# Performance work log

Hardware: AMD Instinct MI355X
Metric: run time of the kernel (lower is better)

Reference implementation:

```python
import jax, jax.numpy as jnp
import numpy as np

M = 1536   # rows (users)
N = 1536   # cols (items)
P_ROW = 4  # Chebyshev order over rows
P_COL = 4  # Chebyshev order over cols
OUT = 32   # out_channels_GCCN


def cheb_basis(L, order):
    """Stack of Chebyshev polynomials T_k(L), shape (order+1, n, n)."""
    n = L.shape[0]
    Ts = [jnp.eye(n, dtype=L.dtype)]
    if order > 0:
        Ts.append(L)
    for _ in range(2, order + 1):
        Ts.append(2.0 * (L @ Ts[-1]) - Ts[-2])
    return jnp.stack(Ts)


def setup_inputs() -> dict:
    key = jax.random.key(0)
    kx, kr, kc, kt = jax.random.split(key, 4)
    x = jax.random.normal(kx, (1, M, N), dtype=jnp.float32)
    # Scaled symmetric 'Laplacians' with spectral radius < 1 so the
    # Chebyshev recursion stays numerically stable.
    Ar = jax.random.normal(kr, (M, M), dtype=jnp.float32)
    Lr = (Ar + Ar.T) / (4.0 * jnp.sqrt(jnp.float32(M)))
    Ac = jax.random.normal(kc, (N, N), dtype=jnp.float32)
    Lc = (Ac + Ac.T) / (4.0 * jnp.sqrt(jnp.float32(N)))
    theta = jax.random.normal(kt, (P_ROW + 1, P_COL + 1, 1, OUT), dtype=jnp.float32) * 0.05
    bias = jnp.zeros((OUT,), dtype=jnp.float32)
    return {"x": x, "Lr": Lr, "Lc": Lc, "theta": theta, "bias": bias}


def reference(x, Lr, Lc, theta, bias):
    # Chebyshev bases: Tr (p_row+1, M, M), Tc (p_col+1, N, N)
    Tr = cheb_basis(Lr, theta.shape[0] - 1)
    Tc = cheb_basis(Lc, theta.shape[1] - 1)
    # Stage 1: row transform -> (i, c, M, N)
    x_row = jnp.einsum('imp,cpn->icmn', Tr, x)
    # Stage 2: col transform -> (i, j, c, M, N)
    basis_feats = jnp.einsum('icmn,jnk->ijcmk', x_row, Tc)
    # Stage 3: bilinear weights -> (OUT, M, N)
    out = jnp.einsum('ijcmn,ijco->omn', basis_feats, theta)
    return out + bias[:, None, None]
```

## Files before the change

kernel.cpp:

```cpp
#include <hip/hip_runtime.h>
#include <hip/hip_bf16.h>


#define NDIM 1536
#define PM (NDIM * NDIM)
#define NK 24

typedef __attribute__((ext_vector_type(8))) short bf16x8;
typedef __attribute__((ext_vector_type(4))) float f32x4;

__device__ inline void gload_lds16(const void* g, void* l) {
  __builtin_amdgcn_global_load_lds(
      (const __attribute__((address_space(1))) void*)g,
      (__attribute__((address_space(3))) void*)l, 16, 0, 0);
}

__device__ inline unsigned short f2bf(float f) {
  __hip_bfloat16 h = __float2bfloat16(f);
  return *reinterpret_cast<unsigned short*>(&h);
}
__device__ inline float bf2f(unsigned short u) {
  return __uint_as_float((unsigned)u << 16);
}

struct ZSet {
  const unsigned short* A;
  const unsigned short* Bt;
  unsigned short* out;
  const unsigned short* Cp;
  int mode;
};
struct ZSet4 { ZSet z[4]; };

#define PH_MID()                                       \
  do {                                                 \
    asm volatile("" ::: "memory");                     \
    __builtin_amdgcn_s_barrier();                      \
    asm volatile("s_waitcnt lgkmcnt(0)" ::: "memory"); \
    __builtin_amdgcn_sched_barrier(0);                 \
    __builtin_amdgcn_s_setprio(1);                     \
  } while (0)

#define PH_END()                                       \
  do {                                                 \
    __builtin_amdgcn_s_setprio(0);                     \
    asm volatile("" ::: "memory");                     \
    __builtin_amdgcn_s_barrier();                      \
  } while (0)

__global__ __launch_bounds__(512, 2) void gemm256_k(ZSet4 zs) {
  const ZSet zp = zs.z[blockIdx.z];
  __shared__ __align__(16) unsigned short As[2][2][8192];
  __shared__ __align__(16) unsigned short Bs[2][2][8192];
  const int tid = threadIdx.x;
  const int lane = tid & 63;
  const int wave = tid >> 6;
  const int wm = wave >> 2, wn = wave & 3;
  const int gm0 = blockIdx.y * 256;
  const int jn = blockIdx.x / 6;
  const int nloc0 = (blockIdx.x % 6) * 256;
  const int q = lane >> 4;
  const int rowl = lane & 15;
  const unsigned short* Ab = zp.A;
  const unsigned short* Btb = zp.Bt + (size_t)jn * PM;
  unsigned short* outb = zp.out + (size_t)jn * 5 * PM;

  bf16x8 a[4][2];
  bf16x8 b0[2][2], b1[2][2];
  f32x4 acc00[4][2] = {}, acc01[4][2] = {}, acc10[4][2] = {}, acc11[4][2] = {};

  auto stageA = [&](int buf, int h, int kt) {
#pragma unroll
    for (int l = 0; l < 2; ++l) {
      const int o = (wave * 2 + l) * 1024 + lane * 16;
      const int wms = o >> 13;
      const int r = (o >> 7) & 63;
      const int s = (o >> 4) & 7;
      const unsigned short* src =
          Ab + (size_t)(gm0 + wms * 128 + h * 64 + r) * NDIM + kt * 64 +
          ((s ^ (r & 7)) << 3);
      gload_lds16(src, &As[buf][h][(wave * 2 + l) * 512]);
    }
  };
  auto stageB = [&](int buf, int h, int kt) {
#pragma unroll
    for (int l = 0; l < 2; ++l) {
      const int o = (wave * 2 + l) * 1024 + lane * 16;
      const int wns = o >> 12;
      const int r = (o >> 7) & 31;
      const int s = (o >> 4) & 7;
      const unsigned short* src =
          Btb + (size_t)(nloc0 + wns * 64 + h * 32 + r) * NDIM + kt * 64 +
          ((s ^ (r & 7)) << 3);
      gload_lds16(src, &Bs[buf][h][(wave * 2 + l) * 512]);
    }
  };
  auto loadA = [&](int buf, int h) {
#pragma unroll
    for (int mt = 0; mt < 4; ++mt) {
      const int lr = mt * 16 + rowl;
#pragma unroll
      for (int ks = 0; ks < 2; ++ks) {
        const int s0 = ks * 4 + q;
        a[mt][ks] = *(const bf16x8*)&As[buf][h][wm * 4096 + lr * 64 +
                                                ((s0 ^ (lr & 7)) << 3)];
      }
    }
  };
  auto loadB = [&](bf16x8 (&bb)[2][2], int buf, int h) {
#pragma unroll
    for (int nt = 0; nt < 2; ++nt) {
      const int lr = nt * 16 + rowl;
#pragma unroll
      for (int ks = 0; ks < 2; ++ks) {
        const int s0 = ks * 4 + q;
        bb[nt][ks] = *(const bf16x8*)&Bs[buf][h][wn * 2048 + lr * 64 +
                                                 ((s0 ^ (lr & 7)) << 3)];
      }
    }
  };
  auto mfma16 = [&](f32x4 (&ac)[4][2], bf16x8 (&bb)[2][2]) {
#pragma unroll
    for (int mt = 0; mt < 4; ++mt)
#pragma unroll
      for (int nt = 0; nt < 2; ++nt)
#pragma unroll
        for (int ks = 0; ks < 2; ++ks)
          ac[mt][nt] = __builtin_amdgcn_mfma_f32_16x16x32_bf16(
              a[mt][ks], bb[nt][ks], ac[mt][nt], 0, 0, 0);
  };

  stageA(0, 0, 0); stageB(0, 0, 0); stageB(0, 1, 0); stageA(0, 1, 0);
  stageA(1, 0, 1); stageB(1, 0, 1); stageB(1, 1, 1);
  asm volatile("s_waitcnt vmcnt(6)" ::: "memory");
  __builtin_amdgcn_s_barrier();

  auto ktile = [&](int kt, int b) {
    loadA(b, 0);
    loadB(b0, b, 0);
    if (kt + 1 < NK) stageA(b ^ 1, 1, kt + 1);
    PH_MID();
    mfma16(acc00, b0);
    PH_END();
    loadB(b1, b, 1);
    if (kt + 2 < NK) stageA(b, 0, kt + 2);
    PH_MID();
    mfma16(acc01, b1);
    PH_END();
    loadA(b, 1);
    if (kt + 2 < NK) stageB(b, 0, kt + 2);
    PH_MID();
    mfma16(acc11, b1);
    PH_END();
    if (kt + 2 < NK) {
      stageB(b, 1, kt + 2);
      asm volatile("s_waitcnt vmcnt(6)" ::: "memory");
    } else {
      asm volatile("s_waitcnt vmcnt(0)" ::: "memory");
    }
    PH_MID();
    mfma16(acc10, b0);
    PH_END();
  };
  for (int kt = 0; kt < NK; kt += 2) {
    ktile(kt, 0);
    ktile(kt + 1, 1);
  }

  auto writeQ = [&](f32x4 (&ac)[4][2], int mh, int nh) {
#pragma unroll
    for (int mt = 0; mt < 4; ++mt)
#pragma unroll
      for (int nt = 0; nt < 2; ++nt)
#pragma unroll
        for (int v = 0; v < 4; ++v) {
          const int row = gm0 + wm * 128 + mh * 64 + mt * 16 + q * 4 + v;
          const int col = nloc0 + wn * 64 + nh * 32 + nt * 16 + rowl;
          const size_t idx = (size_t)row * NDIM + col;
          float val = ac[mt][nt][v];
          if (zp.mode == 1) val = 2.0f * val - bf2f(zp.Cp[idx]);
          if (zp.mode == 2) val = 2.0f * val - (row == col ? 1.0f : 0.0f);
          outb[idx] = f2bf(val);
        }
  };
  writeQ(acc00, 0, 0);
  writeQ(acc01, 0, 1);
  writeQ(acc11, 1, 1);
  writeQ(acc10, 1, 0);
}

__global__ __launch_bounds__(256) void gemm_k(ZSet4 zs) {
  const ZSet zp = zs.z[blockIdx.z];
  __shared__ __align__(16) unsigned short As[128 * 32];
  __shared__ __align__(16) unsigned short Bs[128 * 32];
  const int tid = threadIdx.x;
  const int lane = tid & 63;
  const int wave = tid >> 6;
  const int wm = wave >> 1, wn = wave & 1;
  const int gm0 = blockIdx.y * 128;
  const int jn = blockIdx.x / 12;
  const int nloc0 = (blockIdx.x % 12) * 128;
  const int q = lane >> 4;
  const int rowl = lane & 15;

  const unsigned short* Btb = zp.Bt + (size_t)jn * PM;
  unsigned short* outb = zp.out + (size_t)jn * 5 * PM;

  f32x4 acc[4][4] = {};

  for (int k0 = 0; k0 < NDIM; k0 += 32) {
#pragma unroll
    for (int l = 0; l < 2; ++l) {
      int f = l * 256 + wave * 64 + lane;
      int r = f >> 2, kc = f & 3;
      const unsigned short* ga = zp.A + (size_t)(gm0 + r) * NDIM + k0 + kc * 8;
      const unsigned short* gb = Btb + (size_t)(nloc0 + r) * NDIM + k0 + kc * 8;
      unsigned short* la = &As[(size_t)(l * 256 + wave * 64) * 8];
      unsigned short* lb = &Bs[(size_t)(l * 256 + wave * 64) * 8];
      gload_lds16(ga, la);
      gload_lds16(gb, lb);
    }
    __syncthreads();
    bf16x8 af[4], bfv[4];
#pragma unroll
    for (int t = 0; t < 4; ++t) {
      af[t] = *(const bf16x8*)&As[(wm * 64 + t * 16 + rowl) * 32 + q * 8];
      bfv[t] = *(const bf16x8*)&Bs[(wn * 64 + t * 16 + rowl) * 32 + q * 8];
    }
#pragma unroll
    for (int mt = 0; mt < 4; ++mt)
#pragma unroll
      for (int nt = 0; nt < 4; ++nt)
        acc[mt][nt] = __builtin_amdgcn_mfma_f32_16x16x32_bf16(
            af[mt], bfv[nt], acc[mt][nt], 0, 0, 0);
    __syncthreads();
  }

#pragma unroll
  for (int mt = 0; mt < 4; ++mt) {
#pragma unroll
    for (int nt = 0; nt < 4; ++nt) {
#pragma unroll
      for (int v = 0; v < 4; ++v) {
        int row = gm0 + wm * 64 + mt * 16 + q * 4 + v;
        int col = nloc0 + wn * 64 + nt * 16 + rowl;
        size_t idx = (size_t)row * NDIM + col;
        float val = acc[mt][nt][v];
        if (zp.mode == 1) val = 2.0f * val - bf2f(zp.Cp[idx]);
        if (zp.mode == 2) val = 2.0f * val - (row == col ? 1.0f : 0.0f);
        outb[idx] = f2bf(val);
      }
    }
  }
}

__global__ void transpose_f2b(const float* __restrict__ in,
                              unsigned short* __restrict__ out16,
                              unsigned short* __restrict__ outS) {
  __shared__ float tile[32][33];
  int bx = blockIdx.x, by = blockIdx.y;
  int tx = threadIdx.x;
#pragma unroll
  for (int r = threadIdx.y; r < 32; r += 8) {
    float v = in[(size_t)(by * 32 + r) * NDIM + bx * 32 + tx];
    tile[r][tx] = v;
    outS[(size_t)(by * 32 + r) * NDIM + bx * 32 + tx] = f2bf(v);
  }
  __syncthreads();
  int ox = by * 32 + tx;
#pragma unroll
  for (int r = threadIdx.y; r < 32; r += 8)
    out16[(size_t)(bx * 32 + r) * NDIM + ox] = f2bf(tile[tx][r]);
}

__global__ void cast2_bf16_k(const float* __restrict__ inA,
                             unsigned short* __restrict__ outA,
                             const float* __restrict__ inB,
                             unsigned short* __restrict__ outB) {
  const float* in = blockIdx.y ? inB : inA;
  unsigned short* out = blockIdx.y ? outB : outA;
  int i = (blockIdx.x * 256 + threadIdx.x) * 4;
  float4 v = *(const float4*)(in + i);
  ushort4 r;
  r.x = f2bf(v.x); r.y = f2bf(v.y); r.z = f2bf(v.z); r.w = f2bf(v.w);
  *(ushort4*)(out + i) = r;
}

__global__ __launch_bounds__(256) void combine_k(
    const unsigned short* __restrict__ Z,
    const float* __restrict__ theta,
    const float* __restrict__ bias,
    float* __restrict__ out) {
  __shared__ float th[800];
  __shared__ float bs[32];
  const int tid = threadIdx.x;
  for (int t = tid; t < 800; t += 256) th[t] = theta[t];
  if (tid < 32) bs[tid] = bias[tid];
  __syncthreads();

  const size_t p0 = (size_t)(blockIdx.x * 256 + tid) * 4;
  uint2 zr[25];
#pragma unroll
  for (int c = 0; c < 25; ++c)
    zr[c] = *(const uint2*)(Z + (size_t)c * PM + p0);

#pragma unroll 4
  for (int o = 0; o < 32; ++o) {
    float b = bs[o];
    float a0 = b, a1 = b, a2 = b, a3 = b;
#pragma unroll
    for (int c = 0; c < 25; ++c) {
      const int i = c % 5, j = c / 5;
      float t = th[i * 160 + j * 32 + o];
      a0 += t * __uint_as_float(zr[c].x << 16);
      a1 += t * __uint_as_float(zr[c].x & 0xffff0000u);
      a2 += t * __uint_as_float(zr[c].y << 16);
      a3 += t * __uint_as_float(zr[c].y & 0xffff0000u);
    }
    f32x4 w = {a0, a1, a2, a3};
    __builtin_nontemporal_store(w, (f32x4*)(out + (size_t)o * PM + p0));
  }
}

extern "C" void kernel_launch(void* const* d_in, const int* in_sizes, int n_in,
                              void* d_out, int out_size, void* d_ws, size_t ws_size,
                              hipStream_t stream) {
  (void)in_sizes; (void)n_in; (void)out_size; (void)ws_size;
  const float* X = (const float*)d_in[0];
  const float* Lr = (const float*)d_in[1];
  const float* Lc = (const float*)d_in[2];
  const float* theta = (const float*)d_in[3];
  const float* bias = (const float*)d_in[4];
  float* out = (float*)d_out;

  unsigned short* Zall = (unsigned short*)d_ws;
  unsigned short* Tr = Zall + (size_t)25 * PM;
  unsigned short* Tc = Tr + (size_t)4 * PM;
  unsigned short* Xt = Tc + (size_t)4 * PM;

  unsigned short* Tr0 = Tr;                 unsigned short* Tc0 = Tc;
  unsigned short* Tr1 = Tr + (size_t)PM;    unsigned short* Tc1 = Tc + (size_t)PM;
  unsigned short* Tr2 = Tr + (size_t)2*PM;  unsigned short* Tc2 = Tc + (size_t)2*PM;
  unsigned short* Tr3 = Tr + (size_t)3*PM;  unsigned short* Tc3 = Tc + (size_t)3*PM;

  cast2_bf16_k<<<dim3(PM / 1024, 2), 256, 0, stream>>>(Lr, Tr0, Lc, Tc0);
  transpose_f2b<<<dim3(48, 48), dim3(32, 8), 0, stream>>>(X, Xt, Zall);

  {
    ZSet4 a{};
    a.z[0] = {Tr0, Tr0, Tr1, nullptr, 2};
    a.z[1] = {Tc0, Tc0, Tc1, nullptr, 2};
    gemm_k<<<dim3(12, 12, 2), 256, 0, stream>>>(a);
  }
  {
    ZSet4 a{};
    a.z[0] = {Tr0, Tr1, Tr2, Tr0, 1};
    a.z[1] = {Tr1, Tr1, Tr3, nullptr, 2};
    a.z[2] = {Tc0, Tc1, Tc2, Tc0, 1};
    a.z[3] = {Tc1, Tc1, Tc3, nullptr, 2};
    gemm_k<<<dim3(12, 12, 4), 256, 0, stream>>>(a);
  }
  {
    ZSet4 a{};
    a.z[0] = {Tr, Xt, Zall + (size_t)PM, nullptr, 0};
    gemm256_k<<<dim3(6, 24, 1), 512, 0, stream>>>(a);
  }
  {
    ZSet4 a{};
    a.z[0] = {Zall, Tc0, Zall + (size_t)5 * PM, nullptr, 0};
    gemm256_k<<<dim3(24, 30, 1), 512, 0, stream>>>(a);
  }

  combine_k<<<PM / 1024, 256, 0, stream>>>(Zall, theta, bias, out);
}
```

Measured before the change: 659.2 us.

## Merge second Chebyshev step and first row transform into one launch

Moves the T2/T3 basis GEMMs from the 128-tile gemm_k onto the 256-tile gemm256_k. They now run in the same launch as the row transform of x by T0/T1, which is independent of T2/T3. The remaining row transform by T2/T3 becomes its own launch. A per-set row-block count lets launches with mismatched shapes share one grid, and blocks past that count exit early. The goal is better GPU fill and fewer serial launches, at the cost of idle early-exit blocks and mixed workloads in a single grid.

```diff
diff --git a/kernel.cpp b/kernel.cpp
--- a/kernel.cpp
+++ b/kernel.cpp
@@ -29,8 +29,10 @@
   unsigned short* out;
   const unsigned short* Cp;
   int mode;
+  int mby;
 };
 struct ZSet4 { ZSet z[4]; };
+struct ZSet8 { ZSet z[8]; };
 
 #define PH_MID()                                       \
   do {                                                 \
@@ -48,8 +50,9 @@
     __builtin_amdgcn_s_barrier();                      \
   } while (0)
 
-__global__ __launch_bounds__(512, 2) void gemm256_k(ZSet4 zs) {
+__global__ __launch_bounds__(512, 2) void gemm256_k(ZSet8 zs) {
   const ZSet zp = zs.z[blockIdx.z];
+  if ((int)blockIdx.y >= zp.mby) return;
   __shared__ __align__(16) unsigned short As[2][2][8192];
   __shared__ __align__(16) unsigned short Bs[2][2][8192];
   const int tid = threadIdx.x;
@@ -348,26 +351,27 @@
 
   {
     ZSet4 a{};
-    a.z[0] = {Tr0, Tr0, Tr1, nullptr, 2};
-    a.z[1] = {Tc0, Tc0, Tc1, nullptr, 2};
+    a.z[0] = {Tr0, Tr0, Tr1, nullptr, 2, 12};
+    a.z[1] = {Tc0, Tc0, Tc1, nullptr, 2, 12};
     gemm_k<<<dim3(12, 12, 2), 256, 0, stream>>>(a);
   }
   {
-    ZSet4 a{};
-    a.z[0] = {Tr0, Tr1, Tr2, Tr0, 1};
-    a.z[1] = {Tr1, Tr1, Tr3, nullptr, 2};
-    a.z[2] = {Tc0, Tc1, Tc2, Tc0, 1};
-    a.z[3] = {Tc1, Tc1, Tc3, nullptr, 2};
-    gemm_k<<<dim3(12, 12, 4), 256, 0, stream>>>(a);
+    ZSet8 a{};
+    a.z[0] = {Tr0, Xt, Zall + (size_t)PM, nullptr, 0, 12};
+    a.z[1] = {Tr0, Tr1, Tr2, Tr0, 1, 6};
+    a.z[2] = {Tr1, Tr1, Tr3, nullptr, 2, 6};
+    a.z[3] = {Tc0, Tc1, Tc2, Tc0, 1, 6};
+    a.z[4] = {Tc1, Tc1, Tc3, nullptr, 2, 6};
+    gemm256_k<<<dim3(6, 12, 5), 512, 0, stream>>>(a);
   }
   {
-    ZSet4 a{};
-    a.z[0] = {Tr, Xt, Zall + (size_t)PM, nullptr, 0};
-    gemm256_k<<<dim3(6, 24, 1), 512, 0, stream>>>(a);
+    ZSet8 a{};
+    a.z[0] = {Tr2, Xt, Zall + (size_t)3 * PM, nullptr, 0, 12};
+    gemm256_k<<<dim3(6, 12, 1), 512, 0, stream>>>(a);
   }
   {
-    ZSet4 a{};
-    a.z[0] = {Zall, Tc0, Zall + (size_t)5 * PM, nullptr, 0};
+    ZSet8 a{};
+    a.z[0] = {Zall, Tc0, Zall + (size_t)5 * PM, nullptr, 0, 30};
     gemm256_k<<<dim3(24, 30, 1), 512, 0, stream>>>(a);
   }
 
```

Result: no change. 660.1 us (+0.1%).
